# Kernel tuning notes

Measured on AMD Instinct MI355X. Metric: run time of the kernel, lower is better.

Reference implementation:

```python
import jax, jax.numpy as jnp
import numpy as np


def setup_inputs() -> dict:
    key = jax.random.key(0)
    k1, k2 = jax.random.split(key)
    A, B, N, M, K = 8, 16, 1024, 1024, 64
    u = jax.random.normal(k1, (A, B, N, K), dtype=jnp.float32)
    v = jax.random.normal(k2, (A, B, M, K), dtype=jnp.float32)
    return {"u": u, "v": v}


def reference(u, v):
    # to_norm = u @ v^T has shape (A,B,N,M); we only need its row/col sums.
    # sum over M of (u @ v^T) = u @ sum_m(v);  sum over N = v @ sum_n(u).
    v_sum = v.sum(axis=2)                     # (A,B,K)
    u_sum = u.sum(axis=2)                     # (A,B,K)
    row_sum = jnp.einsum('abnk,abk->abn', u, v_sum)   # to_norm.sum(dim=3)
    col_sum = jnp.einsum('abmk,abk->abm', v, u_sum)   # to_norm.sum(dim=2)
    left_mul = jax.nn.relu(jnp.sign(row_sum))[..., None]   # (A,B,N,1)
    right_mul = jax.nn.relu(jnp.sign(col_sum))[..., None]  # (A,B,M,1)
    return (left_mul * u, right_mul * v)
```

## Files before the change

kernel.cpp:

```cpp
#include <hip/hip_runtime.h>


#define NBATCH 128
#define NROW   1024
#define KDIM   64
#define NPART  8
#define ELEMS_PER_TENSOR (128ull * 1024ull * 64ull)

typedef float floatx4 __attribute__((ext_vector_type(4)));

__global__ __launch_bounds__(256)
void sums_kernel(const float* __restrict__ u,
                 const float* __restrict__ v,
                 float* __restrict__ sums) {
    int bid    = blockIdx.x;
    int batch  = bid >> 3;
    int part   = bid & 7;
    int rstart = part * 128;
    int tid = threadIdx.x;
    int k4  = tid & 15;
    int rg  = tid >> 4;

    const float4* ub = (const float4*)(u + ((size_t)batch * NROW + rstart) * KDIM);
    const float4* vb = (const float4*)(v + ((size_t)batch * NROW + rstart) * KDIM);

    float4 su = make_float4(0.f, 0.f, 0.f, 0.f);
    float4 sv = make_float4(0.f, 0.f, 0.f, 0.f);
    #pragma unroll
    for (int i = 0; i < 8; ++i) {
        int r = rg + 16 * i;
        float4 a = ub[r * 16 + k4];
        float4 b = vb[r * 16 + k4];
        su.x += a.x; su.y += a.y; su.z += a.z; su.w += a.w;
        sv.x += b.x; sv.y += b.y; sv.z += b.z; sv.w += b.w;
    }

    __shared__ float4 lu[16][16];
    __shared__ float4 lv[16][16];
    lu[rg][k4] = su;
    lv[rg][k4] = sv;
    __syncthreads();

    if (tid < 32) {
        int which = tid >> 4;
        int c     = tid & 15;
        float4 t = make_float4(0.f, 0.f, 0.f, 0.f);
        if (which == 0) {
            #pragma unroll
            for (int i = 0; i < 16; ++i) {
                float4 b = lv[i][c];
                t.x += b.x; t.y += b.y; t.z += b.z; t.w += b.w;
            }
        } else {
            #pragma unroll
            for (int i = 0; i < 16; ++i) {
                float4 a = lu[i][c];
                t.x += a.x; t.y += a.y; t.z += a.z; t.w += a.w;
            }
        }
        float* dst = sums + (((size_t)(batch * NPART + part) * 2 + which) * KDIM) + c * 4;
        *(float4*)dst = t;
    }
}

__global__ __launch_bounds__(256)
void mask_kernel(const float* __restrict__ u,
                 const float* __restrict__ v,
                 const float* __restrict__ sums,
                 float* __restrict__ out) {
    int bid  = blockIdx.x;
    int is_v = bid >> 13;
    int lb   = bid & 8191;
    const float* src = is_v ? v : u;
    float* dst = out + (size_t)is_v * ELEMS_PER_TENSOR;

    int batch = lb >> 6;
    int row0  = (lb & 63) * 16;
    int tid   = threadIdx.x;

    __shared__ float s_lds[KDIM];
    if (tid < KDIM) {
        const float* p0 = sums + ((size_t)(batch * NPART) * 2 + is_v) * KDIM + tid;
        float acc = 0.f;
        #pragma unroll
        for (int p = 0; p < NPART; ++p) acc += p0[p * 2 * KDIM];
        s_lds[tid] = acc;
    }
    __syncthreads();

    int k4 = tid & 15;
    int r  = row0 + (tid >> 4);

    size_t off = ((size_t)batch * NROW + r) * KDIM + (size_t)k4 * 4;
    float4 x   = *(const float4*)(src + off);
    float4 sv4 = *(const float4*)(s_lds + k4 * 4);

    float p = x.x * sv4.x + x.y * sv4.y + x.z * sv4.z + x.w * sv4.w;
    p += __shfl_xor(p, 1);
    p += __shfl_xor(p, 2);
    p += __shfl_xor(p, 4);
    p += __shfl_xor(p, 8);

    float m = (p > 0.f) ? 1.f : 0.f;
    floatx4 o = { x.x * m, x.y * m, x.z * m, x.w * m };
    __builtin_nontemporal_store(o, (floatx4*)(dst + off));
}

extern "C" void kernel_launch(void* const* d_in, const int* in_sizes, int n_in,
                              void* d_out, int out_size, void* d_ws, size_t ws_size,
                              hipStream_t stream) {
    const float* u = (const float*)d_in[0];
    const float* v = (const float*)d_in[1];
    float* out  = (float*)d_out;
    float* sums = (float*)d_ws;

    sums_kernel<<<dim3(1024), dim3(256), 0, stream>>>(u, v, sums);
    mask_kernel<<<dim3(16384), dim3(256), 0, stream>>>(u, v, sums, out);
}
```

Measured before the change: 118.7 us.

## Fuse column-sum and mask kernels into one per-batch split kernel

Replaces the two-kernel scheme (partial sums to workspace, then mask) with one kernel. Each block keeps half of one tensor's rows in registers, sums the other tensor for the same batch itself, and writes the masked output. This removes the second launch and the workspace round trip. In exchange it reads the other tensor redundantly across blocks and runs with fewer, larger blocks.

```diff
diff --git a/kernel.cpp b/kernel.cpp
--- a/kernel.cpp
+++ b/kernel.cpp
@@ -4,106 +4,80 @@
 #define NBATCH 128
 #define NROW   1024
 #define KDIM   64
-#define NPART  8
 #define ELEMS_PER_TENSOR (128ull * 1024ull * 64ull)
 
 typedef float floatx4 __attribute__((ext_vector_type(4)));
 
-__global__ __launch_bounds__(256)
-void sums_kernel(const float* __restrict__ u,
-                 const float* __restrict__ v,
-                 float* __restrict__ sums) {
-    int bid    = blockIdx.x;
-    int batch  = bid >> 3;
-    int part   = bid & 7;
-    int rstart = part * 128;
-    int tid = threadIdx.x;
-    int k4  = tid & 15;
-    int rg  = tid >> 4;
+__global__ __launch_bounds__(512)
+void fused_split_kernel(const float* __restrict__ u,
+                        const float* __restrict__ v,
+                        float* __restrict__ out) {
+    const int bid    = blockIdx.x;
+    const int batch  = bid >> 2;
+    const int tensor = (bid >> 1) & 1;
+    const int half   = bid & 1;
+    const int tid    = threadIdx.x;
+    const int k4     = tid & 15;
+    const int rg     = tid >> 4;
+    const int wave   = tid >> 6;
 
-    const float4* ub = (const float4*)(u + ((size_t)batch * NROW + rstart) * KDIM);
-    const float4* vb = (const float4*)(v + ((size_t)batch * NROW + rstart) * KDIM);
+    const float* own_p = tensor ? v : u;
+    const float* oth_p = tensor ? u : v;
+    const float4* ob = (const float4*)(own_p + (size_t)batch * NROW * KDIM);
+    const float4* xb = (const float4*)(oth_p + (size_t)batch * NROW * KDIM);
 
-    float4 su = make_float4(0.f, 0.f, 0.f, 0.f);
-    float4 sv = make_float4(0.f, 0.f, 0.f, 0.f);
+    const int r_own0 = half * 512 + rg;
+    float4 mine[16];
     #pragma unroll
-    for (int i = 0; i < 8; ++i) {
-        int r = rg + 16 * i;
-        float4 a = ub[r * 16 + k4];
-        float4 b = vb[r * 16 + k4];
-        su.x += a.x; su.y += a.y; su.z += a.z; su.w += a.w;
-        sv.x += b.x; sv.y += b.y; sv.z += b.z; sv.w += b.w;
+    for (int i = 0; i < 16; ++i) {
+        mine[i] = ob[(size_t)(r_own0 + 32 * i) * 16 + k4];
     }
 
-    __shared__ float4 lu[16][16];
-    __shared__ float4 lv[16][16];
-    lu[rg][k4] = su;
-    lv[rg][k4] = sv;
+    float4 so = make_float4(0.f, 0.f, 0.f, 0.f);
+    #pragma unroll
+    for (int j = 0; j < 32; ++j) {
+        float4 a = xb[(size_t)(rg + 32 * j) * 16 + k4];
+        so.x += a.x; so.y += a.y; so.z += a.z; so.w += a.w;
+    }
+
+    so.x += __shfl_xor(so.x, 16); so.y += __shfl_xor(so.y, 16);
+    so.z += __shfl_xor(so.z, 16); so.w += __shfl_xor(so.w, 16);
+    so.x += __shfl_xor(so.x, 32); so.y += __shfl_xor(so.y, 32);
+    so.z += __shfl_xor(so.z, 32); so.w += __shfl_xor(so.w, 32);
+
+    __shared__ float4 red[8][16];
+    __shared__ float4 fsum[16];
+    if ((tid & 63) < 16) red[wave][k4] = so;
     __syncthreads();
 
-    if (tid < 32) {
-        int which = tid >> 4;
-        int c     = tid & 15;
+    if (tid < 16) {
         float4 t = make_float4(0.f, 0.f, 0.f, 0.f);
-        if (which == 0) {
-            #pragma unroll
-            for (int i = 0; i < 16; ++i) {
-                float4 b = lv[i][c];
-                t.x += b.x; t.y += b.y; t.z += b.z; t.w += b.w;
-            }
-        } else {
-            #pragma unroll
-            for (int i = 0; i < 16; ++i) {
-                float4 a = lu[i][c];
-                t.x += a.x; t.y += a.y; t.z += a.z; t.w += a.w;
-            }
+        #pragma unroll
+        for (int i = 0; i < 8; ++i) {
+            float4 a = red[i][tid];
+            t.x += a.x; t.y += a.y; t.z += a.z; t.w += a.w;
         }
-        float* dst = sums + (((size_t)(batch * NPART + part) * 2 + which) * KDIM) + c * 4;
-        *(float4*)dst = t;
-    }
-}
-
-__global__ __launch_bounds__(256)
-void mask_kernel(const float* __restrict__ u,
-                 const float* __restrict__ v,
-                 const float* __restrict__ sums,
-                 float* __restrict__ out) {
-    int bid  = blockIdx.x;
-    int is_v = bid >> 13;
-    int lb   = bid & 8191;
-    const float* src = is_v ? v : u;
-    float* dst = out + (size_t)is_v * ELEMS_PER_TENSOR;
-
-    int batch = lb >> 6;
-    int row0  = (lb & 63) * 16;
-    int tid   = threadIdx.x;
-
-    __shared__ float s_lds[KDIM];
-    if (tid < KDIM) {
-        const float* p0 = sums + ((size_t)(batch * NPART) * 2 + is_v) * KDIM + tid;
-        float acc = 0.f;
-        #pragma unroll
-        for (int p = 0; p < NPART; ++p) acc += p0[p * 2 * KDIM];
-        s_lds[tid] = acc;
+        fsum[tid] = t;
     }
     __syncthreads();
 
-    int k4 = tid & 15;
-    int r  = row0 + (tid >> 4);
+    const float4 cs = fsum[k4];
 
-    size_t off = ((size_t)batch * NROW + r) * KDIM + (size_t)k4 * 4;
-    float4 x   = *(const float4*)(src + off);
-    float4 sv4 = *(const float4*)(s_lds + k4 * 4);
-
-    float p = x.x * sv4.x + x.y * sv4.y + x.z * sv4.z + x.w * sv4.w;
-    p += __shfl_xor(p, 1);
-    p += __shfl_xor(p, 2);
-    p += __shfl_xor(p, 4);
-    p += __shfl_xor(p, 8);
-
-    float m = (p > 0.f) ? 1.f : 0.f;
-    floatx4 o = { x.x * m, x.y * m, x.z * m, x.w * m };
-    __builtin_nontemporal_store(o, (floatx4*)(dst + off));
+    float* dst = out + (size_t)tensor * ELEMS_PER_TENSOR
+                     + (size_t)batch * NROW * KDIM;
+    #pragma unroll
+    for (int i = 0; i < 16; ++i) {
+        size_t io = (size_t)(r_own0 + 32 * i) * 16 + k4;
+        float p = mine[i].x * cs.x + mine[i].y * cs.y
+                + mine[i].z * cs.z + mine[i].w * cs.w;
+        p += __shfl_xor(p, 1);
+        p += __shfl_xor(p, 2);
+        p += __shfl_xor(p, 4);
+        p += __shfl_xor(p, 8);
+        float m = (p > 0.f) ? 1.f : 0.f;
+        floatx4 o = { mine[i].x * m, mine[i].y * m, mine[i].z * m, mine[i].w * m };
+        __builtin_nontemporal_store(o, (floatx4*)(dst + io * 4));
+    }
 }
 
 extern "C" void kernel_launch(void* const* d_in, const int* in_sizes, int n_in,
@@ -111,9 +85,7 @@
                               hipStream_t stream) {
     const float* u = (const float*)d_in[0];
     const float* v = (const float*)d_in[1];
-    float* out  = (float*)d_out;
-    float* sums = (float*)d_ws;
+    float* out = (float*)d_out;
 
-    sums_kernel<<<dim3(1024), dim3(256), 0, stream>>>(u, v, sums);
-    mask_kernel<<<dim3(16384), dim3(256), 0, stream>>>(u, v, sums, out);
+    fused_split_kernel<<<dim3(512), dim3(512), 0, stream>>>(u, v, out);
 }
```

Result: slower. 127.8 us (+7.7%).
